# Kernel tuning notes

Measured on AMD Instinct MI355X. Metric: run time of the kernel, lower is better.

The kernel has to match this reference:

```python
import jax, jax.numpy as jnp
import numpy as np

N_EMBED = 2048
N_HEAD = 2
HEAD_SIZE = N_EMBED // N_HEAD  # 1024; mask constraint requires T <= HEAD_SIZE


def setup_inputs() -> dict:
    key = jax.random.key(0)
    ks = jax.random.split(key, 9)
    B, T, C, H, D = 32, 1024, N_EMBED, N_HEAD, HEAD_SIZE
    s = 1.0 / np.sqrt(C)
    x = jax.random.normal(ks[0], (B, T, C), dtype=jnp.float32)
    # torch Linear convention: weight (out_features, in_features), y = x @ W.T + b
    Wq = jax.random.normal(ks[1], (H, D, C), dtype=jnp.float32) * s
    Wk = jax.random.normal(ks[2], (H, D, C), dtype=jnp.float32) * s
    Wv = jax.random.normal(ks[3], (H, D, C), dtype=jnp.float32) * s
    bq = jax.random.normal(ks[4], (H, D), dtype=jnp.float32) * 0.01
    bk = jax.random.normal(ks[5], (H, D), dtype=jnp.float32) * 0.01
    bv = jax.random.normal(ks[6], (H, D), dtype=jnp.float32) * 0.01
    Wo = jax.random.normal(ks[7], (C, H * D), dtype=jnp.float32) * s  # no bias
    return {"x": x, "Wq": Wq, "bq": bq, "Wk": Wk, "bk": bk, "Wv": Wv, "bv": bv, "Wo": Wo}


def reference(x, Wq, bq, Wk, bk, Wv, bv, Wo):
    B, T, C = x.shape
    # per-head projections, batched over heads: (B,T,C) x (H,D,C) -> (B,H,T,D)
    q = jnp.einsum('btc,hdc->bhtd', x, Wq) + bq[None, :, None, :]
    k = jnp.einsum('btc,hdc->bhtd', x, Wk) + bk[None, :, None, :]
    v = jnp.einsum('btc,hdc->bhtd', x, Wv) + bv[None, :, None, :]
    # NOTE: original scales by x.shape[-1]**-0.5 == n_embed**-0.5 (not head_size)
    scale = jnp.asarray(C, x.dtype) ** -0.5
    wei = jnp.einsum('bhtd,bhsd->bhts', q, k) * scale  # (B,H,T,T)
    causal = jnp.tril(jnp.ones((T, T), dtype=bool))
    wei = jnp.where(causal[None, None], wei, -jnp.inf)
    wei = jax.nn.softmax(wei, axis=-1)
    out = jnp.einsum('bhts,bhsd->bhtd', wei, v)  # (B,H,T,D)
    # concat heads along last dim: (B,T,H*D)
    out = out.transpose(0, 2, 1, 3).reshape(B, T, -1)
    return out @ Wo.T  # (B,T,C)
```

## Files before the change

kernel.cpp:

```cpp
#include <hip/hip_runtime.h>
#include <hip/hip_bf16.h>
#include <stdint.h>

typedef __bf16 bf16_t;
typedef __bf16 bf16x8 __attribute__((ext_vector_type(8)));
typedef float f32x4 __attribute__((ext_vector_type(4)));

#define AS1(p) ((const __attribute__((address_space(1))) void*)(uintptr_t)(p))
#define AS3(p) ((__attribute__((address_space(3))) void*)(uintptr_t)(p))

__device__ __forceinline__ void gload16(const bf16_t* g, bf16_t* l) {
  __builtin_amdgcn_global_load_lds(AS1(g), AS3(l), 16, 0, 0);
}

#define SB()      __builtin_amdgcn_sched_barrier(0);
#define BARR()    { __builtin_amdgcn_s_barrier(); __builtin_amdgcn_sched_barrier(0); }
#define VMCNT(n)  { asm volatile("s_waitcnt vmcnt(" #n ")" ::: "memory"); __builtin_amdgcn_sched_barrier(0); }
#define LGKM(n)   { asm volatile("s_waitcnt lgkmcnt(" #n ")" ::: "memory"); __builtin_amdgcn_sched_barrier(0); }

__device__ __forceinline__ void gemm256(const bf16_t* __restrict__ A, int lda,
                                        const bf16_t* __restrict__ B, int ldb,
                                        int nt, f32x4 acc[8][4], bf16_t* lds) {
  const int t = (int)threadIdx.x;
  const int lane = t & 63, wv = t >> 6;
  const int wr = wv >> 2, wc = wv & 3;
  const int fr = lane & 15, fq = lane >> 4;
  char* ldsb = (char*)lds;

  const int s0 = (t * 16) ^ (((t >> 3) & 7) << 4);
  const int r0 = s0 >> 6, q0 = (s0 >> 4) & 3;
  const bf16_t* gA0 = A + (size_t)r0 * lda + q0 * 8;
  const bf16_t* gA1 = gA0 + (size_t)128 * lda;
  const bf16_t* gB0 = B + (size_t)r0 * ldb + q0 * 8;
  const bf16_t* gB1 = gB0 + (size_t)128 * ldb;

  const int swz = (fr * 64 + fq * 16) ^ (((fr >> 1) & 7) << 4);
  const int abase = wr * 8192 + swz;
  const int bbase = 32768 + wc * 4096 + swz;

  bf16x8 bb[4], aa0[4], aa1[4];

#define STAGE_A(cb, kh, kof) { \
    bf16_t* _d = lds + (cb) * 32768 + (kh) * 8192; \
    gload16(gA0 + (kof) + (kh) * 32, _d + t * 8); \
    gload16(gA1 + (kof) + (kh) * 32, _d + 4096 + t * 8); \
  } SB()
#define STAGE_B(cb, kh, kof) { \
    bf16_t* _d = lds + (cb) * 32768 + 16384 + (kh) * 8192; \
    gload16(gB0 + (kof) + (kh) * 32, _d + t * 8); \
    gload16(gB1 + (kof) + (kh) * 32, _d + 4096 + t * 8); \
  } SB()
#define READ_B(cb, kh) { \
    const char* _b = ldsb + (cb) * 65536 + (kh) * 16384 + bbase; \
    _Pragma("unroll") for (int n = 0; n < 4; ++n) bb[n] = *(const bf16x8*)(_b + n * 1024); }
#define READ_A(cb, kh, qm, dst) { \
    const char* _a = ldsb + (cb) * 65536 + (kh) * 16384 + abase + (qm) * 4096; \
    _Pragma("unroll") for (int i = 0; i < 4; ++i) dst[i] = *(const bf16x8*)(_a + i * 1024); }
#define MFMA16(dst, qm) { \
    __builtin_amdgcn_s_setprio(1); \
    _Pragma("unroll") for (int i = 0; i < 4; ++i) \
      _Pragma("unroll") for (int n = 0; n < 4; ++n) \
        acc[(qm) * 4 + i][n] = __builtin_amdgcn_mfma_f32_16x16x32_bf16(dst[i], bb[n], acc[(qm) * 4 + i][n], 0, 0, 0); \
    __builtin_amdgcn_s_setprio(0); }

  STAGE_A(0, 0, 0) STAGE_B(0, 0, 0) STAGE_A(0, 1, 0) STAGE_B(0, 1, 0)

  int kof = 64;
  for (int tt = 0; tt < nt - 1; ++tt, kof += 64) {
    const int cb = tt & 1;
    VMCNT(4) BARR()
    READ_B(cb, 0) READ_A(cb, 0, 0, aa0)
    STAGE_A(cb ^ 1, 0, kof)
    READ_A(cb, 0, 1, aa1)
    STAGE_B(cb ^ 1, 0, kof)
    LGKM(4) MFMA16(aa0, 0)
    LGKM(0) MFMA16(aa1, 1)
    VMCNT(4) BARR()
    READ_B(cb, 1) READ_A(cb, 1, 0, aa0)
    STAGE_A(cb ^ 1, 1, kof)
    READ_A(cb, 1, 1, aa1)
    STAGE_B(cb ^ 1, 1, kof)
    LGKM(4) MFMA16(aa0, 0)
    LGKM(0) MFMA16(aa1, 1)
  }
  {
    const int cb = (nt - 1) & 1;
    VMCNT(4) BARR()
    READ_B(cb, 0) READ_A(cb, 0, 0, aa0) READ_A(cb, 0, 1, aa1)
    LGKM(4) MFMA16(aa0, 0)
    LGKM(0) MFMA16(aa1, 1)
    VMCNT(0) BARR()
    READ_B(cb, 1) READ_A(cb, 1, 0, aa0) READ_A(cb, 1, 1, aa1)
    LGKM(4) MFMA16(aa0, 0)
    LGKM(0) MFMA16(aa1, 1)
  }
#undef STAGE_A
#undef STAGE_B
#undef READ_B
#undef READ_A
#undef MFMA16
}

#define EPI_VARS \
  const int t = (int)threadIdx.x; \
  const int lane = t & 63, w = t >> 6; \
  const int wr = w >> 2, wc = w & 3; \
  const int fr = lane & 15, fq = lane >> 4;

#define ZERO8x4(acc) \
  _Pragma("unroll") for (int _i = 0; _i < 8; ++_i) \
  _Pragma("unroll") for (int _j = 0; _j < 4; ++_j) { f32x4 _z = {0.f,0.f,0.f,0.f}; acc[_i][_j] = _z; }

__global__ void k_cvt(const float* __restrict__ s, bf16_t* __restrict__ d, long n8) {
  long i = (long)blockIdx.x * blockDim.x + threadIdx.x;
  long st = (long)gridDim.x * blockDim.x;
  for (; i < n8; i += st) {
    const float4* sp = (const float4*)(s + i * 8);
    float4 a = sp[0], b = sp[1];
    bf16x8 v;
    v[0] = (__bf16)a.x; v[1] = (__bf16)a.y; v[2] = (__bf16)a.z; v[3] = (__bf16)a.w;
    v[4] = (__bf16)b.x; v[5] = (__bf16)b.y; v[6] = (__bf16)b.z; v[7] = (__bf16)b.w;
    *(bf16x8*)(d + i * 8) = v;
  }
}

__global__ void k_cvtw(const float* __restrict__ Wq, const float* __restrict__ Wk,
                       const float* __restrict__ Wv, const float* __restrict__ Wo,
                       bf16_t* __restrict__ d) {
  long i = (long)blockIdx.x * blockDim.x + threadIdx.x;
  long st = (long)gridDim.x * blockDim.x;
  for (; i < 2097152L; i += st) {
    int r = (int)(i >> 19);
    const float* s = (r == 0 ? Wq : r == 1 ? Wk : r == 2 ? Wv : Wo) + (i & 524287L) * 8;
    float4 a = ((const float4*)s)[0], b = ((const float4*)s)[1];
    bf16x8 v;
    v[0] = (__bf16)a.x; v[1] = (__bf16)a.y; v[2] = (__bf16)a.z; v[3] = (__bf16)a.w;
    v[4] = (__bf16)b.x; v[5] = (__bf16)b.y; v[6] = (__bf16)b.z; v[7] = (__bf16)b.w;
    *(bf16x8*)(d + i * 8) = v;
  }
}

__global__ void k_fill(float* o, float v, long n) {
  long i = (long)blockIdx.x * blockDim.x + threadIdx.x;
  long st = (long)gridDim.x * blockDim.x;
  for (; i < n; i += st) o[i] = v;
}

__global__ __launch_bounds__(512, 2) void k_qkv256(
    const bf16_t* __restrict__ xb, const bf16_t* __restrict__ Wb,
    const float* __restrict__ bq, const float* __restrict__ bk, const float* __restrict__ bv,
    bf16_t* __restrict__ Q, bf16_t* __restrict__ K, bf16_t* __restrict__ Vt) {
  __shared__ __align__(16) bf16_t lds[65536];
  int bid = (int)blockIdx.x;
  int id = (bid & 7) * 384 + (bid >> 3);
  EPI_VARS
  f32x4 acc[8][4];
  ZERO8x4(acc)

  bool vmode = id >= 2048;
  int mt = 0, ntile = 0, tok = 0, wm = 0;
  const bf16_t *Ap, *Bp;
  if (!vmode) {
    mt = id & 127; ntile = id >> 7;
    Ap = xb + (size_t)mt * 256 * 2048;
    Bp = Wb + (size_t)ntile * 256 * 2048;
  } else {
    int vb = id - 2048;
    tok = vb & 127; wm = vb >> 7;
    Ap = Wb + (size_t)(16 + wm) * 256 * 2048;
    Bp = xb + (size_t)tok * 256 * 2048;
  }
  gemm256(Ap, 2048, Bp, 2048, 32, acc, lds);

  if (!vmode) {
    int sel = ntile >> 3;
    const float* bias = sel ? bk : bq;
    bf16_t* dst = sel ? K : Q;
    int cbase = (ntile & 7) * 256 + wc * 64;
#pragma unroll
    for (int ni = 0; ni < 4; ++ni) {
      int c2 = cbase + ni * 16 + fr;
      int h = c2 >> 10, d = c2 & 1023;
      float bb = bias[c2];
#pragma unroll
      for (int mi = 0; mi < 8; ++mi) {
        f32x4 a = acc[mi][ni];
#pragma unroll
        for (int r = 0; r < 4; ++r) {
          int m = mt * 256 + wr * 128 + mi * 16 + fq * 4 + r;
          int b = m >> 10, tk = m & 1023;
          dst[(((size_t)(b * 2 + h) << 10) + tk) * 1024 + d] = (bf16_t)(a[r] + bb);
        }
      }
    }
  } else {
#pragma unroll
    for (int mi = 0; mi < 8; ++mi) {
#pragma unroll
      for (int r = 0; r < 4; ++r) {
        int gd = wm * 256 + wr * 128 + mi * 16 + fq * 4 + r;
        int h = gd >> 10, dd = gd & 1023;
        float bb = bv[gd];
#pragma unroll
        for (int ni = 0; ni < 4; ++ni) {
          int m = tok * 256 + wc * 64 + ni * 16 + fr;
          int b = m >> 10, tk = m & 1023;
          Vt[(((size_t)(b * 2 + h) << 10) + dd) * 1024 + tk] = (bf16_t)(acc[mi][ni][r] + bb);
        }
      }
    }
  }
}

__global__ __launch_bounds__(512, 2) void k_s256(const bf16_t* __restrict__ Q,
                                                 const bf16_t* __restrict__ K,
                                                 bf16_t* __restrict__ S, int pbase) {
  __shared__ __align__(16) bf16_t lds[65536];
  int id = (int)blockIdx.x;
  int pc = id / 10, rem = id % 10;
  int ti = 0;
  while (rem > ti) { rem -= ti + 1; ++ti; }
  int tj = rem;
  size_t p = (size_t)(pbase + pc);
  EPI_VARS
  f32x4 acc[8][4];
  ZERO8x4(acc)
  gemm256(Q + (p << 20) + (size_t)ti * 256 * 1024, 1024,
          K + (p << 20) + (size_t)tj * 256 * 1024, 1024, 16, acc, lds);
  bf16_t* Sp = S + ((size_t)pc << 20);
  const float scale = 0.022097086912079608f;
#pragma unroll
  for (int mi = 0; mi < 8; ++mi)
#pragma unroll
    for (int ni = 0; ni < 4; ++ni) {
      int col = tj * 256 + wc * 64 + ni * 16 + fr;
      f32x4 a = acc[mi][ni];
#pragma unroll
      for (int r = 0; r < 4; ++r) {
        int row = ti * 256 + wr * 128 + mi * 16 + fq * 4 + r;
        Sp[((size_t)row << 10) + col] = (bf16_t)(a[r] * scale);
      }
    }
}

__global__ __launch_bounds__(256) void k_softmax(const bf16_t* __restrict__ S,
                                                 bf16_t* __restrict__ P) {
  int gw = (int)blockIdx.x * 4 + ((int)threadIdx.x >> 6);
  int pc = gw >> 10, row = gw & 1023;
  int lane = (int)threadIdx.x & 63;
  const bf16_t* s = S + ((size_t)pc << 20) + ((size_t)row << 10);
  bf16_t* p = P + ((size_t)pc << 20) + ((size_t)row << 10);
  int cend = ((row >> 8) + 1) << 8;
  bf16x8 v0 = *(const bf16x8*)(s + lane * 8);
  bf16x8 v1 = *(const bf16x8*)(s + 512 + lane * 8);
  float x[16];
  float mx = -1e30f;
#pragma unroll
  for (int j = 0; j < 8; ++j) {
    int c0 = lane * 8 + j, c1 = 512 + lane * 8 + j;
    x[j]     = (c0 <= row) ? (float)v0[j] : -1e30f;
    x[8 + j] = (c1 <= row) ? (float)v1[j] : -1e30f;
    mx = fmaxf(mx, fmaxf(x[j], x[8 + j]));
  }
  for (int o = 32; o > 0; o >>= 1) mx = fmaxf(mx, __shfl_xor(mx, o));
  float sum = 0.f;
#pragma unroll
  for (int j = 0; j < 16; ++j) {
    x[j] = (x[j] > -1e29f) ? __expf(x[j] - mx) : 0.f;
    sum += x[j];
  }
  for (int o = 32; o > 0; o >>= 1) sum += __shfl_xor(sum, o);
  float inv = 1.f / sum;
  bf16x8 o0, o1;
#pragma unroll
  for (int j = 0; j < 8; ++j) {
    o0[j] = (bf16_t)(x[j] * inv);
    o1[j] = (bf16_t)(x[8 + j] * inv);
  }
  if (lane * 8 < cend)       *(bf16x8*)(p + lane * 8) = o0;
  if (512 + lane * 8 < cend) *(bf16x8*)(p + 512 + lane * 8) = o1;
}

__global__ __launch_bounds__(512, 2) void k_pv256(const bf16_t* __restrict__ P,
                                                  const bf16_t* __restrict__ Vt,
                                                  bf16_t* __restrict__ O, int pbase) {
  __shared__ __align__(16) bf16_t lds[65536];
  int id = (int)blockIdx.x;
  int pc = id >> 4, rem = id & 15;
  int ti = rem >> 2, dj = rem & 3;
  size_t p = (size_t)(pbase + pc);
  EPI_VARS
  f32x4 acc[8][4];
  ZERO8x4(acc)
  gemm256(P + ((size_t)pc << 20) + (size_t)ti * 256 * 1024, 1024,
          Vt + (p << 20) + (size_t)dj * 256 * 1024, 1024, (ti + 1) * 4, acc, lds);
  int b = (int)(p >> 1), h = (int)(p & 1);
#pragma unroll
  for (int mi = 0; mi < 8; ++mi)
#pragma unroll
    for (int ni = 0; ni < 4; ++ni) {
      int dcol = dj * 256 + wc * 64 + ni * 16 + fr;
      f32x4 a = acc[mi][ni];
#pragma unroll
      for (int r = 0; r < 4; ++r) {
        int tk = ti * 256 + wr * 128 + mi * 16 + fq * 4 + r;
        O[(((size_t)b << 10) + tk) * 2048 + (h << 10) + dcol] = (bf16_t)a[r];
      }
    }
}

__global__ __launch_bounds__(512, 2) void k_out256(const bf16_t* __restrict__ O,
                                                   const bf16_t* __restrict__ W,
                                                   float* __restrict__ out) {
  __shared__ __align__(16) bf16_t lds[65536];
  int bid = (int)blockIdx.x;
  int id = (bid & 7) * 128 + (bid >> 3);
  int mt = id & 127, ntile = id >> 7;
  EPI_VARS
  f32x4 acc[8][4];
  ZERO8x4(acc)
  gemm256(O + (size_t)mt * 256 * 2048, 2048, W + (size_t)ntile * 256 * 2048, 2048, 32, acc, lds);
#pragma unroll
  for (int mi = 0; mi < 8; ++mi)
#pragma unroll
    for (int ni = 0; ni < 4; ++ni) {
      int col = ntile * 256 + wc * 64 + ni * 16 + fr;
      f32x4 a = acc[mi][ni];
#pragma unroll
      for (int r = 0; r < 4; ++r) {
        int row = mt * 256 + wr * 128 + mi * 16 + fq * 4 + r;
        out[(size_t)row * 2048 + col] = a[r];
      }
    }
}

extern "C" void kernel_launch(void* const* d_in, const int* in_sizes, int n_in,
                              void* d_out, int out_size, void* d_ws, size_t ws_size,
                              hipStream_t stream) {
  const float* x  = (const float*)d_in[0];
  const float* Wq = (const float*)d_in[1];
  const float* bq = (const float*)d_in[2];
  const float* Wk = (const float*)d_in[3];
  const float* bk = (const float*)d_in[4];
  const float* Wv = (const float*)d_in[5];
  const float* bv = (const float*)d_in[6];
  const float* Wo = (const float*)d_in[7];
  float* out = (float*)d_out;

  const size_t MiB = 1ull << 20;
  char* w = (char*)d_ws;
  bf16_t* xb    = (bf16_t*)w;
  bf16_t* Ob    = xb;
  bf16_t* Qb    = (bf16_t*)(w + 128 * MiB);
  bf16_t* Kb    = (bf16_t*)(w + 256 * MiB);
  bf16_t* Vt    = (bf16_t*)(w + 384 * MiB);
  bf16_t* Wqkvb = (bf16_t*)(w + 512 * MiB);
  bf16_t* Wob   = (bf16_t*)(w + 536 * MiB);
  bf16_t* Sc    = (bf16_t*)(w + 544 * MiB);

  size_t rem = ws_size > 544 * MiB ? ws_size - 544 * MiB : 0;
  int NP = (int)(rem / (2 * MiB));
  if (NP > 64) NP = 64;
  if (NP < 1) {
    k_fill<<<2048, 256, 0, stream>>>(out, (float)(ws_size >> 20), (long)out_size);
    return;
  }

  k_cvt<<<2048, 256, 0, stream>>>(x, xb, 8388608L);
  k_cvtw<<<2048, 256, 0, stream>>>(Wq, Wk, Wv, Wo, Wqkvb);

  k_qkv256<<<3072, 512, 0, stream>>>(xb, Wqkvb, bq, bk, bv, Qb, Kb, Vt);

  for (int base = 0; base < 64; base += NP) {
    int np = (64 - base) < NP ? (64 - base) : NP;
    k_s256<<<np * 10, 512, 0, stream>>>(Qb, Kb, Sc, base);
    k_softmax<<<np * 256, 256, 0, stream>>>(Sc, Sc);
    k_pv256<<<np * 16, 512, 0, stream>>>(Sc, Vt, Ob, base);
  }

  k_out256<<<1024, 512, 0, stream>>>(Ob, Wob, out);
}
```

Before: 1.475 ms.

## Restructure GEMM mainloop into 4-slot ring buffer with 3-deep prefetch

Replaces the double-buffered 64-wide K tile pipeline (two half-stages per tile) with a 4-slot ring of 32-wide K windows, keeping three windows in flight ahead of compute. Each window stages A and B together and is consumed after a single barrier, with vmcnt waits adjusted to 8/4/0 in the drain. This aims to hide more global-load latency behind MFMA work, at the cost of the same LDS footprint but deeper outstanding loads and more complex wait accounting.

New measurement: 1.492 ms. Within noise of the previous version (+1.2%).

```diff
diff --git a/kernel.cpp b/kernel.cpp
--- a/kernel.cpp
+++ b/kernel.cpp
@@ -36,25 +36,22 @@
 
   const int swz = (fr * 64 + fq * 16) ^ (((fr >> 1) & 7) << 4);
   const int abase = wr * 8192 + swz;
-  const int bbase = 32768 + wc * 4096 + swz;
+  const int bbase = 16384 + wc * 4096 + swz;
 
   bf16x8 bb[4], aa0[4], aa1[4];
 
-#define STAGE_A(cb, kh, kof) { \
-    bf16_t* _d = lds + (cb) * 32768 + (kh) * 8192; \
-    gload16(gA0 + (kof) + (kh) * 32, _d + t * 8); \
-    gload16(gA1 + (kof) + (kh) * 32, _d + 4096 + t * 8); \
+#define STAGE(sl, kof) { \
+    bf16_t* _d = lds + (sl) * 16384; \
+    gload16(gA0 + (kof), _d + t * 8); \
+    gload16(gA1 + (kof), _d + 4096 + t * 8); \
+    gload16(gB0 + (kof), _d + 8192 + t * 8); \
+    gload16(gB1 + (kof), _d + 12288 + t * 8); \
   } SB()
-#define STAGE_B(cb, kh, kof) { \
-    bf16_t* _d = lds + (cb) * 32768 + 16384 + (kh) * 8192; \
-    gload16(gB0 + (kof) + (kh) * 32, _d + t * 8); \
-    gload16(gB1 + (kof) + (kh) * 32, _d + 4096 + t * 8); \
-  } SB()
-#define READ_B(cb, kh) { \
-    const char* _b = ldsb + (cb) * 65536 + (kh) * 16384 + bbase; \
+#define READ_B(sl) { \
+    const char* _b = ldsb + (sl) * 32768 + bbase; \
     _Pragma("unroll") for (int n = 0; n < 4; ++n) bb[n] = *(const bf16x8*)(_b + n * 1024); }
-#define READ_A(cb, kh, qm, dst) { \
-    const char* _a = ldsb + (cb) * 65536 + (kh) * 16384 + abase + (qm) * 4096; \
+#define READ_A(sl, qm, dst) { \
+    const char* _a = ldsb + (sl) * 32768 + abase + (qm) * 4096; \
     _Pragma("unroll") for (int i = 0; i < 4; ++i) dst[i] = *(const bf16x8*)(_a + i * 1024); }
 #define MFMA16(dst, qm) { \
     __builtin_amdgcn_s_setprio(1); \
@@ -62,43 +59,29 @@
       _Pragma("unroll") for (int n = 0; n < 4; ++n) \
         acc[(qm) * 4 + i][n] = __builtin_amdgcn_mfma_f32_16x16x32_bf16(dst[i], bb[n], acc[(qm) * 4 + i][n], 0, 0, 0); \
     __builtin_amdgcn_s_setprio(0); }
-
-  STAGE_A(0, 0, 0) STAGE_B(0, 0, 0) STAGE_A(0, 1, 0) STAGE_B(0, 1, 0)
-
-  int kof = 64;
-  for (int tt = 0; tt < nt - 1; ++tt, kof += 64) {
-    const int cb = tt & 1;
-    VMCNT(4) BARR()
-    READ_B(cb, 0) READ_A(cb, 0, 0, aa0)
-    STAGE_A(cb ^ 1, 0, kof)
-    READ_A(cb, 0, 1, aa1)
-    STAGE_B(cb ^ 1, 0, kof)
-    LGKM(4) MFMA16(aa0, 0)
+#define WINDOW_BODY(sl, DOSTAGE) \
+    READ_B(sl) READ_A(sl, 0, aa0) \
+    DOSTAGE \
+    READ_A(sl, 1, aa1) \
+    LGKM(4) MFMA16(aa0, 0) \
     LGKM(0) MFMA16(aa1, 1)
-    VMCNT(4) BARR()
-    READ_B(cb, 1) READ_A(cb, 1, 0, aa0)
-    STAGE_A(cb ^ 1, 1, kof)
-    READ_A(cb, 1, 1, aa1)
-    STAGE_B(cb ^ 1, 1, kof)
-    LGKM(4) MFMA16(aa0, 0)
-    LGKM(0) MFMA16(aa1, 1)
-  }
-  {
-    const int cb = (nt - 1) & 1;
-    VMCNT(4) BARR()
-    READ_B(cb, 0) READ_A(cb, 0, 0, aa0) READ_A(cb, 0, 1, aa1)
-    LGKM(4) MFMA16(aa0, 0)
-    LGKM(0) MFMA16(aa1, 1)
-    VMCNT(0) BARR()
-    READ_B(cb, 1) READ_A(cb, 1, 0, aa0) READ_A(cb, 1, 1, aa1)
-    LGKM(4) MFMA16(aa0, 0)
-    LGKM(0) MFMA16(aa1, 1)
-  }
-#undef STAGE_A
-#undef STAGE_B
+
+  const int H = nt * 2;
+  STAGE(0, 0) STAGE(1, 32) STAGE(2, 64)
+  int kof = 96;
+  for (int w = 0; w + 3 < H; ++w, kof += 32) {
+    const int sl = w & 3;
+    VMCNT(8) BARR()
+    WINDOW_BODY(sl, STAGE((w + 3) & 3, kof))
+  }
+  { const int sl = (H - 3) & 3; VMCNT(8) BARR() WINDOW_BODY(sl, ) }
+  { const int sl = (H - 2) & 3; VMCNT(4) BARR() WINDOW_BODY(sl, ) }
+  { const int sl = (H - 1) & 3; VMCNT(0) BARR() WINDOW_BODY(sl, ) }
+#undef STAGE
 #undef READ_B
 #undef READ_A
 #undef MFMA16
+#undef WINDOW_BODY
 }
 
 #define EPI_VARS \
```
